# Performance work log

Hardware: AMD Instinct MI355X
Metric: run time of the kernel (lower is better)

The kernel has to match this reference:

```python
import jax, jax.numpy as jnp
import numpy as np

B, S, D, H = 2, 2048, 1024, 16
DH = D // H  # 64
EPS = 1e-5


def setup_inputs() -> dict:
    key = jax.random.key(0)
    ks = jax.random.split(key, 16)
    s = 0.02
    return {
        "emb": jax.random.normal(ks[0], (B, S, D), dtype=jnp.float32),
        # per-head projections, stacked: torch Linear weight layout [out, in] -> [H, DH, D]
        "Wq": jax.random.normal(ks[1], (H, DH, D), dtype=jnp.float32) * s,
        "bq": jnp.zeros((H, DH), dtype=jnp.float32),
        "Wk": jax.random.normal(ks[2], (H, DH, D), dtype=jnp.float32) * s,
        "bk": jnp.zeros((H, DH), dtype=jnp.float32),
        "Wv": jax.random.normal(ks[3], (H, DH, D), dtype=jnp.float32) * s,
        "bv": jnp.zeros((H, DH), dtype=jnp.float32),
        "W0": jax.random.normal(ks[4], (D, D), dtype=jnp.float32) * s,
        "b0": jnp.zeros((D,), dtype=jnp.float32),
        "g1": jnp.ones((D,), dtype=jnp.float32),
        "be1": jnp.zeros((D,), dtype=jnp.float32),
        "W1": jax.random.normal(ks[5], (4 * D, D), dtype=jnp.float32) * s,
        "b1": jnp.zeros((4 * D,), dtype=jnp.float32),
        "W2": jax.random.normal(ks[6], (D, 4 * D), dtype=jnp.float32) * s,
        "b2": jnp.zeros((D,), dtype=jnp.float32),
        "g2": jnp.ones((D,), dtype=jnp.float32),
        "be2": jnp.zeros((D,), dtype=jnp.float32),
    }


def _layer_norm(x, g, b):
    mu = jnp.mean(x, axis=-1, keepdims=True)
    var = jnp.mean(jnp.square(x - mu), axis=-1, keepdims=True)
    return (x - mu) * jax.lax.rsqrt(var + EPS) * g + b


def reference(emb, Wq, bq, Wk, bk, Wv, bv, W0, b0, g1, be1, W1, b1, W2, b2, g2, be2):
    # per-head Q/K/V projections, batched over heads  -> [B, H, S, DH]
    q = jnp.einsum("bsd,hed->bhse", emb, Wq) + bq[None, :, None, :]
    k = jnp.einsum("bsd,hed->bhse", emb, Wk) + bk[None, :, None, :]
    v = jnp.einsum("bsd,hed->bhse", emb, Wv) + bv[None, :, None, :]
    # NOTE: original module applies NO scale before softmax; it divides the
    # softmax(QK^T) @ V output by sqrt(d_head) afterwards. Kept faithfully.
    scores = jnp.einsum("bhse,bhte->bhst", q, k)  # [B,H,S,S]
    attn = jax.nn.softmax(scores, axis=-1)
    z = jnp.einsum("bhst,bhte->bhse", attn, v) / np.sqrt(DH).astype(np.float32)
    # concat heads along feature dim (head 0 first) -> [B, S, D]
    z = z.transpose(0, 2, 1, 3).reshape(B, S, D)
    z = z @ W0.T + b0
    out1 = _layer_norm(z + emb, g1, be1)
    h = jax.nn.relu(out1 @ W1.T + b1)  # [B, S, 4D]
    out2 = _layer_norm(out1 + (h @ W2.T + b2), g2, be2)
    return out2
```

## Files before the change

### kernel.cpp

```cpp
#include <hip/hip_runtime.h>
#include <hip/hip_bf16.h>
#include <cstdint>
#include <cmath>

#define DEV __device__ __forceinline__

typedef float f32x4 __attribute__((ext_vector_type(4)));
typedef float f32x16 __attribute__((ext_vector_type(16)));
typedef __bf16 bf16x8 __attribute__((ext_vector_type(8)));
typedef unsigned short u16;
typedef u16 u16x8 __attribute__((ext_vector_type(8)));
typedef u16 u16x4 __attribute__((ext_vector_type(4)));

DEV u16 f2bf(float f) {
  union { float f; uint32_t u; } x{f};
  uint32_t r = x.u + 0x7FFFu + ((x.u >> 16) & 1u);
  return (u16)(r >> 16);
}

DEV void gl_lds16(const u16* g, u16* l) {
  __builtin_amdgcn_global_load_lds((const __attribute__((address_space(1))) void*)g,
                                   (__attribute__((address_space(3))) void*)l, 16, 0, 0);
}

__global__ __launch_bounds__(256) void k_cvt_all(
    const float* __restrict__ emb, const float* __restrict__ Wq,
    const float* __restrict__ Wk, const float* __restrict__ Wv,
    const float* __restrict__ W0, const float* __restrict__ W1,
    const float* __restrict__ W2,
    u16* __restrict__ embb, u16* __restrict__ Wqb, u16* __restrict__ Wkb,
    u16* __restrict__ Wvb, u16* __restrict__ W0b, u16* __restrict__ W1b,
    u16* __restrict__ W2b) {
  const int step = gridDim.x * blockDim.x;
  for (int i4 = blockIdx.x * blockDim.x + threadIdx.x; i4 < 4194304; i4 += step) {
    const int i = i4 * 4;
    const float* s; u16* d; int off;
    if (i < 4194304)       { s = emb; d = embb; off = 0; }
    else if (i < 5242880)  { s = Wq;  d = Wqb;  off = 4194304; }
    else if (i < 6291456)  { s = Wk;  d = Wkb;  off = 5242880; }
    else if (i < 7340032)  { s = Wv;  d = Wvb;  off = 6291456; }
    else if (i < 8388608)  { s = W0;  d = W0b;  off = 7340032; }
    else if (i < 12582912) { s = W1;  d = W1b;  off = 8388608; }
    else                   { s = W2;  d = W2b;  off = 12582912; }
    float4 v = *reinterpret_cast<const float4*>(s + (i - off));
    u16x4 o;
    o[0] = f2bf(v.x); o[1] = f2bf(v.y); o[2] = f2bf(v.z); o[3] = f2bf(v.w);
    *reinterpret_cast<u16x4*>(d + (i - off)) = o;
  }
}

template <int MODE>
DEV void gemm_core64(const u16* __restrict__ A, const u16* __restrict__ B,
                     const float* __restrict__ bias,
                     void* __restrict__ C, int N, int K, int KL,
                     int m0, int n0, float oscale) {
  __shared__ u16 sA[2][64 * 32];
  __shared__ u16 sB[2][128 * 32];
  const int tid = threadIdx.x;
  const int w = tid >> 6, l = tid & 63;
  const int lr = l & 15, lg = l >> 4;
  const int wr = (w >> 1) * 32, wc = (w & 1) * 64;

  f32x4 acc[2][4] = {};

  const int nt = KL >> 5;
  const int sr = w * 16 + (l >> 2);
  const int sc = (l & 3) * 8;

  auto stage = [&](int buf, int t) {
    gl_lds16(A + (size_t)(m0 + sr) * K + t * 32 + sc, &sA[buf][w * 512]);
    const u16* gb = B + (size_t)(n0 + sr) * K + t * 32 + sc;
    gl_lds16(gb, &sB[buf][w * 512]);
    gl_lds16(gb + (size_t)64 * K, &sB[buf][2048 + w * 512]);
  };

  auto compute = [&](int buf) {
    bf16x8 af[2], bfr[4];
#pragma unroll
    for (int mf = 0; mf < 2; ++mf)
      af[mf] = *(const bf16x8*)&sA[buf][(wr + mf * 16 + lr) * 32 + lg * 8];
#pragma unroll
    for (int nf = 0; nf < 4; ++nf)
      bfr[nf] = *(const bf16x8*)&sB[buf][(wc + nf * 16 + lr) * 32 + lg * 8];
#pragma unroll
    for (int mf = 0; mf < 2; ++mf)
#pragma unroll
      for (int nf = 0; nf < 4; ++nf)
        acc[mf][nf] = __builtin_amdgcn_mfma_f32_16x16x32_bf16(af[mf], bfr[nf],
                                                              acc[mf][nf], 0, 0, 0);
  };

  stage(0, 0);
  __syncthreads();
  int cur = 0;
  for (int t = 0; t < nt - 1; ++t) {
    stage(cur ^ 1, t + 1);
    compute(cur);
    __syncthreads();
    cur ^= 1;
  }
  compute(cur);

#pragma unroll
  for (int nf = 0; nf < 4; ++nf) {
    const int col = n0 + wc + nf * 16 + lr;
    const float bv = (MODE == 3) ? 0.0f : bias[col];
#pragma unroll
    for (int mf = 0; mf < 2; ++mf) {
      const int row0 = m0 + wr + mf * 16 + lg * 4;
#pragma unroll
      for (int r = 0; r < 4; ++r) {
        float v = acc[mf][nf][r] + bv;
        if (MODE == 0) v *= oscale;
        if (MODE == 1) v = fmaxf(v, 0.0f);
        const size_t idx = (size_t)(row0 + r) * N + col;
        if (MODE == 3) ((float*)C)[idx] = v;
        else ((u16*)C)[idx] = f2bf(v);
      }
    }
  }
}

template <int MODE>
__global__ __launch_bounds__(256) void k_gemm64(const u16* __restrict__ A,
                                                const u16* __restrict__ B,
                                                const float* __restrict__ bias,
                                                void* __restrict__ C, int N, int K) {
  gemm_core64<MODE>(A, B, bias, C, N, K, K, blockIdx.x * 64, blockIdx.y * 128, 1.0f);
}

__global__ __launch_bounds__(256) void k_gemm64sk(const u16* __restrict__ A,
                                                  const u16* __restrict__ B,
                                                  float* __restrict__ C,
                                                  int N, int K, int Kh,
                                                  size_t partStride) {
  const int z = blockIdx.z;
  gemm_core64<3>(A + z * Kh, B + z * Kh, nullptr, C + z * partStride,
                 N, K, Kh, blockIdx.x * 64, blockIdx.y * 128, 1.0f);
}

__global__ __launch_bounds__(256) void k_gemm_qkv(
    const u16* __restrict__ A, const u16* __restrict__ B0, const u16* __restrict__ B1,
    const u16* __restrict__ B2, const float* __restrict__ c0,
    const float* __restrict__ c1, const float* __restrict__ c2,
    u16* __restrict__ O0, u16* __restrict__ O1, u16* __restrict__ O2) {
  const int z = blockIdx.z;
  const u16* B = (z == 0) ? B0 : (z == 1) ? B1 : B2;
  const float* bias = (z == 0) ? c0 : (z == 1) ? c1 : c2;
  u16* O = (z == 0) ? O0 : (z == 1) ? O1 : O2;
  const float sc = (z == 0) ? 1.44269504f : 1.0f;
  gemm_core64<0>(A, B, bias, O, 1024, 1024, 1024, blockIdx.x * 64,
                 blockIdx.y * 128, sc);
}

__global__ __launch_bounds__(256, 4) void k_attn(const u16* __restrict__ Q,
                                                 const u16* __restrict__ K,
                                                 const u16* __restrict__ V,
                                                 float* __restrict__ pz,
                                                 float* __restrict__ pl) {
  const int id = blockIdx.x;
  const int virt = (id & 7) * 128 + (id >> 3);
  const int bh = virt >> 5;
  const int qt = (virt >> 1) & 15;
  const int half = virt & 1;
  const int b = bh >> 4, h = bh & 15;
  const int tid = threadIdx.x;
  const int w = tid >> 6, l = tid & 63;
  const int q32 = l & 31, hi = l >> 5;

  __shared__ u16 Kl[2][4096];
  __shared__ u16 VT[2][4096];

  const size_t rb = (size_t)b * 2048;
  const int c0 = h * 64;
  const int q0w = qt * 128 + w * 32;
  const int t0 = half * 16;

  bf16x8 qb[4];
#pragma unroll
  for (int st = 0; st < 4; ++st)
    qb[st] = *(const bf16x8*)(Q + (rb + q0w + q32) * 1024 + c0 + st * 16 + hi * 8);

  f32x16 zacc[2] = {};
  f32x4 lacc = {};

  const int skv = w * 16 + (l >> 3);
  const int sc8 = l & 7;
  auto stage_k = [&](int pp, int t) {
#pragma unroll
    for (int cq = 0; cq < 2; ++cq) {
      const int kvl = skv + cq * 8;
      const int dh0 = (sc8 ^ (kvl & 7)) * 8;
      gl_lds16(K + (rb + t * 64 + kvl) * 1024 + c0 + dh0,
               &Kl[pp][w * 1024 + cq * 512]);
    }
  };

  const int vp = tid & 31, vd0 = (tid >> 5) * 8;
  u16x8 va0, va1;
  auto vload = [&](int t) {
    const u16* v0 = V + (rb + t * 64 + 2 * vp) * 1024 + c0 + vd0;
    va0 = *(const u16x8*)v0;
    va1 = *(const u16x8*)(v0 + 1024);
  };
  auto vstore = [&](int pp) {
#pragma unroll
    for (int i = 0; i < 8; ++i) {
      const int dh = vd0 + i;
      const int off = ((2 * vp) & 7) + 8 * ((vp >> 2) ^ (dh & 7));
      uint32_t pk = (uint32_t)va0[i] | ((uint32_t)va1[i] << 16);
      *(uint32_t*)&VT[pp][dh * 64 + off] = pk;
    }
  };

  stage_k(0, t0);
  vload(t0);
  vstore(0);
  __syncthreads();

  for (int tt = 0; tt < 16; ++tt) {
    const int bp = tt & 1;
    if (tt + 1 < 16) {
      stage_k(bp ^ 1, t0 + tt + 1);
      vload(t0 + tt + 1);
    }
    f32x16 s[2] = {};
    __builtin_amdgcn_s_setprio(1);
#pragma unroll
    for (int nf = 0; nf < 2; ++nf)
#pragma unroll
      for (int st = 0; st < 4; ++st) {
        bf16x8 ka = *(const bf16x8*)&Kl[bp][(nf * 32 + q32) * 64 +
                                            ((st * 2 + hi) ^ (q32 & 7)) * 8];
        s[nf] = __builtin_amdgcn_mfma_f32_32x32x16_bf16(ka, qb[st], s[nf], 0, 0, 0);
      }
    __builtin_amdgcn_s_setprio(0);

    uint32_t c[16];
#pragma unroll
    for (int nf = 0; nf < 2; ++nf)
#pragma unroll
      for (int m2 = 0; m2 < 8; ++m2) {
        float p0 = exp2f(s[nf][2 * m2]);
        float p1 = exp2f(s[nf][2 * m2 + 1]);
        lacc[m2 & 3] += p0 + p1;
        uint32_t pk;
        asm("v_cvt_pk_bf16_f32 %0, %1, %2" : "=v"(pk) : "v"(p0), "v"(p1));
        c[nf * 8 + m2] = pk;
      }
#pragma unroll
    for (int ks = 0; ks < 4; ++ks) {
      asm("v_permlane32_swap_b32 %0, %1" : "+v"(c[4 * ks]), "+v"(c[4 * ks + 2]));
      asm("v_permlane32_swap_b32 %0, %1" : "+v"(c[4 * ks + 1]), "+v"(c[4 * ks + 3]));
    }

    if (tt + 1 < 16) vstore(bp ^ 1);

    __builtin_amdgcn_s_setprio(1);
#pragma unroll
    for (int ks = 0; ks < 4; ++ks) {
      union { uint32_t u[4]; bf16x8 v; } pa;
#pragma unroll
      for (int i = 0; i < 4; ++i) pa.u[i] = c[4 * ks + i];
#pragma unroll
      for (int nd = 0; nd < 2; ++nd) {
        bf16x8 vb = *(const bf16x8*)&VT[bp][(nd * 32 + q32) * 64 +
                                            ((ks * 2 + hi) ^ (q32 & 7)) * 8];
        zacc[nd] = __builtin_amdgcn_mfma_f32_32x32x16_bf16(pa.v, vb, zacc[nd], 0, 0, 0);
      }
    }
    __builtin_amdgcn_s_setprio(0);
    __syncthreads();
  }

  float* pzb = pz + (size_t)virt * 8192;
#pragma unroll
  for (int r = 0; r < 16; ++r) {
    const int crow = (r & 3) + 8 * (r >> 2) + 4 * hi;
#pragma unroll
    for (int nd = 0; nd < 2; ++nd)
      pzb[(w * 32 + crow) * 64 + nd * 32 + q32] = zacc[nd][r];
  }
  float lrun = (lacc[0] + lacc[1]) + (lacc[2] + lacc[3]);
  float ltot = lrun + __shfl_xor(lrun, 32, 64);
  if (hi == 0) pl[virt * 128 + w * 32 + q32] = ltot;
}

__global__ __launch_bounds__(256) void k_attn_merge(const float* __restrict__ pz,
                                                    const float* __restrict__ pl,
                                                    u16* __restrict__ Z) {
  const int id = blockIdx.x;
  const int virt2 = (id & 7) * 64 + (id >> 3);
  const int bh = virt2 >> 4, qt = virt2 & 15;
  const int b = bh >> 4, h = bh & 15;
  const int va = 2 * virt2;
  const int tid = threadIdx.x;
  const int row = tid >> 1;
  const int col0 = (tid & 1) * 32;

  const float la = pl[va * 128 + row];
  const float lb = pl[(va + 1) * 128 + row];
  const float inv = 0.125f / (la + lb);

  const float* za = pz + (size_t)va * 8192 + row * 64 + col0;
  const float* zb = za + 8192;
  u16* zo = Z + ((size_t)b * 2048 + qt * 128 + row) * 1024 + h * 64 + col0;
#pragma unroll
  for (int e = 0; e < 8; ++e) {
    float4 a = *(const float4*)(za + e * 4);
    float4 bv = *(const float4*)(zb + e * 4);
    u16x4 o;
    o[0] = f2bf((a.x + bv.x) * inv);
    o[1] = f2bf((a.y + bv.y) * inv);
    o[2] = f2bf((a.z + bv.z) * inv);
    o[3] = f2bf((a.w + bv.w) * inv);
    *(u16x4*)(zo + e * 4) = o;
  }
}

template <bool WBF>
__global__ __launch_bounds__(256) void k_ln_merge(const float* __restrict__ pa,
                                                  const float* __restrict__ pb,
                                                  const float* __restrict__ bias,
                                                  const float* __restrict__ res,
                                                  const float* __restrict__ g,
                                                  const float* __restrict__ be,
                                                  float* __restrict__ of,
                                                  u16* __restrict__ ob) {
  const int row = blockIdx.x;
  const int tid = threadIdx.x;
  const size_t base = (size_t)row * 1024 + tid * 4;
  float4 a = *(const float4*)(pa + base);
  float4 b = *(const float4*)(pb + base);
  float4 rr = *(const float4*)(res + base);
  float4 bv = *(const float4*)(bias + tid * 4);
  float4 v;
  v.x = a.x + b.x + rr.x + bv.x;
  v.y = a.y + b.y + rr.y + bv.y;
  v.z = a.z + b.z + rr.z + bv.z;
  v.w = a.w + b.w + rr.w + bv.w;

  float s = v.x + v.y + v.z + v.w;
  float s2 = v.x * v.x + v.y * v.y + v.z * v.z + v.w * v.w;
#pragma unroll
  for (int st = 1; st < 64; st <<= 1) {
    s += __shfl_xor(s, st, 64);
    s2 += __shfl_xor(s2, st, 64);
  }
  __shared__ float ps[8];
  if ((tid & 63) == 0) { ps[tid >> 6] = s; ps[4 + (tid >> 6)] = s2; }
  __syncthreads();
  s = ps[0] + ps[1] + ps[2] + ps[3];
  s2 = ps[4] + ps[5] + ps[6] + ps[7];
  const float mu = s * 0.0009765625f;
  const float var = s2 * 0.0009765625f - mu * mu;
  const float rs = rsqrtf(var + 1e-5f);
  float4 gg = *(const float4*)(g + tid * 4);
  float4 bb = *(const float4*)(be + tid * 4);
  float4 o;
  o.x = (v.x - mu) * rs * gg.x + bb.x;
  o.y = (v.y - mu) * rs * gg.y + bb.y;
  o.z = (v.z - mu) * rs * gg.z + bb.z;
  o.w = (v.w - mu) * rs * gg.w + bb.w;
  *(float4*)(of + (size_t)row * 1024 + tid * 4) = o;
  if (WBF) {
    u16x4 q;
    q[0] = f2bf(o.x); q[1] = f2bf(o.y); q[2] = f2bf(o.z); q[3] = f2bf(o.w);
    *(u16x4*)(ob + (size_t)row * 1024 + tid * 4) = q;
  }
}

extern "C" void kernel_launch(void* const* d_in, const int* in_sizes, int n_in,
                              void* d_out, int out_size, void* d_ws, size_t ws_size,
                              hipStream_t stream) {
  const float* emb = (const float*)d_in[0];
  const float* Wq  = (const float*)d_in[1];
  const float* bq  = (const float*)d_in[2];
  const float* Wk  = (const float*)d_in[3];
  const float* bk  = (const float*)d_in[4];
  const float* Wv  = (const float*)d_in[5];
  const float* bv  = (const float*)d_in[6];
  const float* W0  = (const float*)d_in[7];
  const float* b0  = (const float*)d_in[8];
  const float* g1  = (const float*)d_in[9];
  const float* be1 = (const float*)d_in[10];
  const float* W1  = (const float*)d_in[11];
  const float* b1  = (const float*)d_in[12];
  const float* W2  = (const float*)d_in[13];
  const float* b2  = (const float*)d_in[14];
  const float* g2  = (const float*)d_in[15];
  const float* be2 = (const float*)d_in[16];

  char* p = (char*)d_ws;
  auto alloc = [&](size_t bytes) { char* r = p; p += bytes; return r; };
  u16* embb = (u16*)alloc(8u << 20);
  u16* Wqb  = (u16*)alloc(2u << 20);
  u16* Wkb  = (u16*)alloc(2u << 20);
  u16* Wvb  = (u16*)alloc(2u << 20);
  u16* W0b  = (u16*)alloc(2u << 20);
  u16* W1b  = (u16*)alloc(8u << 20);
  u16* W2b  = (u16*)alloc(8u << 20);
  u16* Qb   = (u16*)alloc(8u << 20);
  u16* Kb   = (u16*)alloc(8u << 20);
  u16* Vb   = (u16*)alloc(8u << 20);
  u16* Zb   = (u16*)alloc(8u << 20);
  float* o1f = (float*)alloc(16u << 20);
  u16* o1b  = (u16*)alloc(8u << 20);
  u16* hb   = (u16*)alloc(32u << 20);
  float* pl = (float*)alloc(1u << 20);

  float* pz = (float*)hb;

  k_cvt_all<<<2048, 256, 0, stream>>>(emb, Wq, Wk, Wv, W0, W1, W2,
                                      embb, Wqb, Wkb, Wvb, W0b, W1b, W2b);

  k_gemm_qkv<<<dim3(64, 8, 3), 256, 0, stream>>>(embb, Wqb, Wkb, Wvb, bq, bk, bv,
                                                 Qb, Kb, Vb);
  k_attn<<<dim3(1024), 256, 0, stream>>>(Qb, Kb, Vb, pz, pl);
  k_attn_merge<<<dim3(512), 256, 0, stream>>>(pz, pl, Zb);

  float* w0p = (float*)hb;
  k_gemm64sk<<<dim3(64, 8, 2), 256, 0, stream>>>(Zb, W0b, w0p, 1024, 1024, 512,
                                                 (size_t)4096 * 1024);
  k_ln_merge<true><<<4096, 256, 0, stream>>>(w0p, w0p + (size_t)4096 * 1024,
                                             b0, emb, g1, be1, o1f, o1b);
  k_gemm64<1><<<dim3(64, 32), 256, 0, stream>>>(o1b, W1b, b1, hb, 4096, 1024);
  float* f2p = (float*)Qb;
  k_gemm64sk<<<dim3(64, 8, 2), 256, 0, stream>>>(hb, W2b, f2p, 1024, 4096, 2048,
                                                 (size_t)4096 * 1024);
  k_ln_merge<false><<<4096, 256, 0, stream>>>(f2p, f2p + (size_t)4096 * 1024,
                                              b2, o1f, g2, be2, (float*)d_out,
                                              nullptr);
}
```

Baseline: 296.1 us.

## Split FFN down-projection K four ways with bf16 partials and fused LN merge

The second FFN GEMM now uses a four-way split-K with partial sums stored as bf16, which doubles the block count and halves the bytes per partial. A new layer-norm kernel sums the four bf16 partials with bias and residual. The attention kernel also uses a byte-permute for the V transpose packing and the raw hardware exp2 builtin. Storing partials in bf16 adds rounding error before the residual and norm.

```diff
diff --git a/kernel.cpp b/kernel.cpp
--- a/kernel.cpp
+++ b/kernel.cpp
@@ -16,6 +16,11 @@
   union { float f; uint32_t u; } x{f};
   uint32_t r = x.u + 0x7FFFu + ((x.u >> 16) & 1u);
   return (u16)(r >> 16);
+}
+
+DEV float b2f(u16 h) {
+  union { uint32_t u; float f; } x{(uint32_t)h << 16};
+  return x.f;
 }
 
 DEV void gl_lds16(const u16* g, u16* l) {
@@ -104,7 +109,7 @@
 #pragma unroll
   for (int nf = 0; nf < 4; ++nf) {
     const int col = n0 + wc + nf * 16 + lr;
-    const float bv = (MODE == 3) ? 0.0f : bias[col];
+    const float bv = (MODE >= 3) ? 0.0f : bias[col];
 #pragma unroll
     for (int mf = 0; mf < 2; ++mf) {
       const int row0 = m0 + wr + mf * 16 + lg * 4;
@@ -129,14 +134,16 @@
   gemm_core64<MODE>(A, B, bias, C, N, K, K, blockIdx.x * 64, blockIdx.y * 128, 1.0f);
 }
 
+template <int MODE>
 __global__ __launch_bounds__(256) void k_gemm64sk(const u16* __restrict__ A,
                                                   const u16* __restrict__ B,
-                                                  float* __restrict__ C,
+                                                  void* __restrict__ C,
                                                   int N, int K, int Kh,
                                                   size_t partStride) {
   const int z = blockIdx.z;
-  gemm_core64<3>(A + z * Kh, B + z * Kh, nullptr, C + z * partStride,
-                 N, K, Kh, blockIdx.x * 64, blockIdx.y * 128, 1.0f);
+  char* Cp = (char*)C + (size_t)z * partStride * ((MODE == 3) ? 4 : 2);
+  gemm_core64<MODE>(A + z * Kh, B + z * Kh, nullptr, Cp,
+                    N, K, Kh, blockIdx.x * 64, blockIdx.y * 128, 1.0f);
 }
 
 __global__ __launch_bounds__(256) void k_gemm_qkv(
@@ -204,11 +211,14 @@
     va1 = *(const u16x8*)(v0 + 1024);
   };
   auto vstore = [&](int pp) {
+    const uint32_t* A0 = (const uint32_t*)&va0;
+    const uint32_t* A1 = (const uint32_t*)&va1;
 #pragma unroll
     for (int i = 0; i < 8; ++i) {
       const int dh = vd0 + i;
       const int off = ((2 * vp) & 7) + 8 * ((vp >> 2) ^ (dh & 7));
-      uint32_t pk = (uint32_t)va0[i] | ((uint32_t)va1[i] << 16);
+      uint32_t pk = __builtin_amdgcn_perm(A1[i >> 1], A0[i >> 1],
+                                          (i & 1) ? 0x07060302u : 0x05040100u);
       *(uint32_t*)&VT[pp][dh * 64 + off] = pk;
     }
   };
@@ -241,8 +251,8 @@
     for (int nf = 0; nf < 2; ++nf)
 #pragma unroll
       for (int m2 = 0; m2 < 8; ++m2) {
-        float p0 = exp2f(s[nf][2 * m2]);
-        float p1 = exp2f(s[nf][2 * m2 + 1]);
+        float p0 = __builtin_amdgcn_exp2f(s[nf][2 * m2]);
+        float p1 = __builtin_amdgcn_exp2f(s[nf][2 * m2 + 1]);
         lacc[m2 & 3] += p0 + p1;
         uint32_t pk;
         asm("v_cvt_pk_bf16_f32 %0, %1, %2" : "=v"(pk) : "v"(p0), "v"(p1));
@@ -370,6 +380,51 @@
   }
 }
 
+__global__ __launch_bounds__(256) void k_ln_merge4(const u16* __restrict__ pp,
+                                                   size_t ps,
+                                                   const float* __restrict__ bias,
+                                                   const float* __restrict__ res,
+                                                   const float* __restrict__ g,
+                                                   const float* __restrict__ be,
+                                                   float* __restrict__ of) {
+  const int row = blockIdx.x;
+  const int tid = threadIdx.x;
+  const size_t base = (size_t)row * 1024 + tid * 4;
+  float4 rr = *(const float4*)(res + base);
+  float4 bv = *(const float4*)(bias + tid * 4);
+  float4 v;
+  v.x = rr.x + bv.x; v.y = rr.y + bv.y; v.z = rr.z + bv.z; v.w = rr.w + bv.w;
+#pragma unroll
+  for (int z = 0; z < 4; ++z) {
+    u16x4 q = *(const u16x4*)(pp + z * ps + base);
+    v.x += b2f(q[0]); v.y += b2f(q[1]); v.z += b2f(q[2]); v.w += b2f(q[3]);
+  }
+
+  float s = v.x + v.y + v.z + v.w;
+  float s2 = v.x * v.x + v.y * v.y + v.z * v.z + v.w * v.w;
+#pragma unroll
+  for (int st = 1; st < 64; st <<= 1) {
+    s += __shfl_xor(s, st, 64);
+    s2 += __shfl_xor(s2, st, 64);
+  }
+  __shared__ float ps2[8];
+  if ((tid & 63) == 0) { ps2[tid >> 6] = s; ps2[4 + (tid >> 6)] = s2; }
+  __syncthreads();
+  s = ps2[0] + ps2[1] + ps2[2] + ps2[3];
+  s2 = ps2[4] + ps2[5] + ps2[6] + ps2[7];
+  const float mu = s * 0.0009765625f;
+  const float var = s2 * 0.0009765625f - mu * mu;
+  const float rs = rsqrtf(var + 1e-5f);
+  float4 gg = *(const float4*)(g + tid * 4);
+  float4 bb = *(const float4*)(be + tid * 4);
+  float4 o;
+  o.x = (v.x - mu) * rs * gg.x + bb.x;
+  o.y = (v.y - mu) * rs * gg.y + bb.y;
+  o.z = (v.z - mu) * rs * gg.z + bb.z;
+  o.w = (v.w - mu) * rs * gg.w + bb.w;
+  *(float4*)(of + (size_t)row * 1024 + tid * 4) = o;
+}
+
 extern "C" void kernel_launch(void* const* d_in, const int* in_sizes, int n_in,
                               void* d_out, int out_size, void* d_ws, size_t ws_size,
                               hipStream_t stream) {
@@ -408,6 +463,7 @@
   u16* o1b  = (u16*)alloc(8u << 20);
   u16* hb   = (u16*)alloc(32u << 20);
   float* pl = (float*)alloc(1u << 20);
+  (void)Kb; (void)Vb;
 
   float* pz = (float*)hb;
 
@@ -420,15 +476,13 @@
   k_attn_merge<<<dim3(512), 256, 0, stream>>>(pz, pl, Zb);
 
   float* w0p = (float*)hb;
-  k_gemm64sk<<<dim3(64, 8, 2), 256, 0, stream>>>(Zb, W0b, w0p, 1024, 1024, 512,
-                                                 (size_t)4096 * 1024);
+  k_gemm64sk<3><<<dim3(64, 8, 2), 256, 0, stream>>>(Zb, W0b, w0p, 1024, 1024, 512,
+                                                    (size_t)4096 * 1024);
   k_ln_merge<true><<<4096, 256, 0, stream>>>(w0p, w0p + (size_t)4096 * 1024,
                                              b0, emb, g1, be1, o1f, o1b);
   k_gemm64<1><<<dim3(64, 32), 256, 0, stream>>>(o1b, W1b, b1, hb, 4096, 1024);
-  float* f2p = (float*)Qb;
-  k_gemm64sk<<<dim3(64, 8, 2), 256, 0, stream>>>(hb, W2b, f2p, 1024, 4096, 2048,
-                                                 (size_t)4096 * 1024);
-  k_ln_merge<false><<<4096, 256, 0, stream>>>(f2p, f2p + (size_t)4096 * 1024,
-                                              b2, o1f, g2, be2, (float*)d_out,
-                                              nullptr);
-}
+  k_gemm64sk<4><<<dim3(64, 8, 4), 256, 0, stream>>>(hb, W2b, Qb, 1024, 4096, 1024,
+                                                    (size_t)4096 * 1024);
+  k_ln_merge4<<<4096, 256, 0, stream>>>(Qb, (size_t)4096 * 1024, b2, o1f,
+                                        g2, be2, (float*)d_out);
+}
```

Result: faster. 288.8 us (-2.5%).
